# Optimization experiments

Hardware: AMD Instinct MI355X
Metric: run time of the kernel (lower is better)

The kernel has to match this reference:

```python
import jax, jax.numpy as jnp
import numpy as np

B, T, D = 4, 2048, 2048
P, K, ALPHA, R = 512, 16, 4, 32
E_RATIO = 0.8
EPS = 1e-6


def rmsnorm(x, g):
    return x * jax.lax.rsqrt(jnp.mean(x * x, axis=-1, keepdims=True) + EPS) * g


def dale_signs():
    # first e_ratio*P neurons excitatory (+1), rest inhibitory (-1)
    return jnp.where(jnp.arange(P) < int(E_RATIO * P), 1.0, -1.0)


def quant_dale(w, signs):
    # STE sign-quantization with per-neuron mean-abs scale + Dale's-law sign constraint
    scale = jnp.mean(jnp.abs(w), axis=-1, keepdims=True)  # [P,1]
    q = scale * signs[:, None] * jnp.ones_like(w)         # magnitude=scale, sign fixed per neuron
    return w + jax.lax.stop_gradient(q - w)


def synapse_graph(x, idx, w):
    # x: [B,T,D], idx: [P,K] int, w: [P,K] -> dendritic inputs [B,T,P,K]
    return jnp.take(x, idx, axis=-1) * w


def perceptron(x_dend, Wp, Wout, signs):
    Wq = quant_dale(Wp, signs)                              # [P,K]
    u = jnp.einsum('btpk,pk->btp', x_dend, Wq)              # [B,T,P]
    f = jax.nn.sigmoid(u)                                   # gate [B,T,P]
    f_out = quant_dale(Wout, signs)                         # [P,ALPHA]
    y = (f * u)[..., None] * f_out                          # [B,T,P,ALPHA]
    return u, f, y, f_out


def low_rank_ssm(t, f, s0, U, V, Wgate, bgate):
    # t,f: [B,T,P]; s0: [B,R]. Low-rank gated linear scan in R dims.
    z = jnp.einsum('btp,pr->btr', t, U)
    lam = jax.nn.sigmoid(jnp.einsum('btp,pr->btr', f, Wgate) + bgate)

    def step(s, inp):
        z_t, l_t = inp
        s = l_t * s + z_t
        return s, s

    sT, S = jax.lax.scan(step, s0, (jnp.moveaxis(z, 1, 0), jnp.moveaxis(lam, 1, 0)))
    tilde = jnp.einsum('btr,rp->btp', jnp.moveaxis(S, 0, 1), V)
    return tilde, sT


def flatten_ports(y):
    return y.reshape(*y.shape[:-2], P * ALPHA)


def setup_inputs() -> dict:
    key = jax.random.key(0)
    ks = jax.random.split(key, 14)
    sc = 0.1
    return {
        'x': jax.random.normal(ks[0], (B, T, D), jnp.float32),
        'state': jnp.zeros((B, R), jnp.float32),
        'g1': jnp.ones((D,), jnp.float32),
        'g2': jnp.ones((D,), jnp.float32),
        'idx_ssm': jax.random.randint(ks[1], (P, K), 0, D),
        'wg_ssm': jax.random.normal(ks[2], (P, K), jnp.float32) * sc,
        'idx_mlp': jax.random.randint(ks[3], (P, K), 0, D),
        'wg_mlp': jax.random.normal(ks[4], (P, K), jnp.float32) * sc,
        'Wp_ssm': jax.random.normal(ks[5], (P, K), jnp.float32) * sc,
        'Wout_ssm': jax.random.normal(ks[6], (P, ALPHA), jnp.float32) * sc,
        'Wp_mlp': jax.random.normal(ks[7], (P, K), jnp.float32) * sc,
        'Wout_mlp': jax.random.normal(ks[8], (P, ALPHA), jnp.float32) * sc,
        'U': jax.random.normal(ks[9], (P, R), jnp.float32) * sc,
        'V': jax.random.normal(ks[10], (R, P), jnp.float32) * sc,
        'Wgate': jax.random.normal(ks[11], (P, R), jnp.float32) * sc,
        'bgate': jnp.zeros((R,), jnp.float32),
    }


def reference(x, state, g1, g2, idx_ssm, wg_ssm, idx_mlp, wg_mlp,
              Wp_ssm, Wout_ssm, Wp_mlp, Wout_mlp, U, V, Wgate, bgate):
    signs = dale_signs()
    # --- SSM branch ---
    h1 = rmsnorm(x, g1)
    x_dend_ssm = synapse_graph(h1, idx_ssm, wg_ssm)
    u_ssm, f_ssm, _, f_out = perceptron(x_dend_ssm, Wp_ssm, Wout_ssm, signs)
    t_ssm = f_ssm * u_ssm
    tilde_t, new_state = low_rank_ssm(t_ssm, f_ssm, state, U, V, Wgate, bgate)
    y_ssm = (f_ssm * tilde_t)[..., None] * f_out            # [B,T,P,ALPHA]
    x_after = x + flatten_ports(y_ssm)
    # --- MLP branch ---
    h2 = rmsnorm(x_after, g2)
    x_dend_mlp = synapse_graph(h2, idx_mlp, wg_mlp)
    _, _, y_mlp, _ = perceptron(x_dend_mlp, Wp_mlp, Wout_mlp, signs)
    x_out = x_after + flatten_ports(y_mlp)
    return x_out, new_state
```

## Files before the change

### kernel.cpp

```cpp
#include <hip/hip_runtime.h>
#include <hip/hip_bf16.h>

#define B_ 4
#define T_ 2048
#define D_ 2048
#define P_ 512
#define K_ 16
#define ALPHA_ 4
#define R_ 32
#define NE_ 409
#define EPS_ 1e-6f
#define G_ 4

typedef unsigned short u16;

__device__ __forceinline__ float sigmoidf_(float x) {
  return 1.0f / (1.0f + __expf(-x));
}
__device__ __forceinline__ float bfb2f(u16 u) {
  return __uint_as_float(((unsigned int)u) << 16);
}
__device__ __forceinline__ u16 f2bfb(float f) {
  __hip_bfloat16 h = __float2bfloat16(f);
  return *reinterpret_cast<u16*>(&h);
}

__global__ void k_scalars(const float* __restrict__ Wp_s, const float* __restrict__ Wo_s,
                          const float* __restrict__ Wp_m, const float* __restrict__ Wo_m,
                          float* __restrict__ wq_s, float* __restrict__ fo_s,
                          float* __restrict__ wq_m, float* __restrict__ fo_m) {
  int p = blockIdx.x * blockDim.x + threadIdx.x;
  if (p >= P_) return;
  float sgn = (p < NE_) ? 1.0f : -1.0f;
  float a = 0, b = 0, c = 0, d = 0;
#pragma unroll
  for (int k = 0; k < K_; k++) {
    a += fabsf(Wp_s[p * K_ + k]);
    c += fabsf(Wp_m[p * K_ + k]);
  }
#pragma unroll
  for (int k = 0; k < ALPHA_; k++) {
    b += fabsf(Wo_s[p * ALPHA_ + k]);
    d += fabsf(Wo_m[p * ALPHA_ + k]);
  }
  wq_s[p] = sgn * a * (1.0f / K_);
  fo_s[p] = sgn * b * (1.0f / ALPHA_);
  wq_m[p] = sgn * c * (1.0f / K_);
  fo_m[p] = sgn * d * (1.0f / ALPHA_);
}

__global__ __launch_bounds__(256) void k_phase1(
    const float* __restrict__ x, const float* __restrict__ g1,
    const int* __restrict__ idx, const float* __restrict__ wg,
    const float* __restrict__ U, const float* __restrict__ Wgt,
    const float* __restrict__ bg, const float* __restrict__ wq,
    float* __restrict__ f_ssm, float* __restrict__ z, float* __restrict__ lam) {
  __shared__ u16 h1[G_][D_];
  __shared__ float fl[G_][P_];
  __shared__ float tl[G_][P_];
  __shared__ float red[G_][4];
  __shared__ float zp[G_][R_][4];
  __shared__ float lp[G_][R_][4];

  int tid = threadIdx.x;
  int token0 = blockIdx.x * G_;
  int b = token0 >> 11;
  int t0 = token0 & (T_ - 1);

  float gv[8];
  {
    const float4* gp = reinterpret_cast<const float4*>(g1 + tid * 8);
    *reinterpret_cast<float4*>(&gv[0]) = gp[0];
    *reinterpret_cast<float4*>(&gv[4]) = gp[1];
  }
  float xv[G_][8];
  float ssv[G_];
#pragma unroll
  for (int tok = 0; tok < G_; tok++) {
    const float4* xp = reinterpret_cast<const float4*>(x + (size_t)(token0 + tok) * D_ + tid * 8);
    *reinterpret_cast<float4*>(&xv[tok][0]) = xp[0];
    *reinterpret_cast<float4*>(&xv[tok][4]) = xp[1];
    float ss = 0;
#pragma unroll
    for (int i = 0; i < 8; i++) ss += xv[tok][i] * xv[tok][i];
    ssv[tok] = ss;
  }
#pragma unroll
  for (int tok = 0; tok < G_; tok++) {
    float s = ssv[tok];
#pragma unroll
    for (int off = 32; off; off >>= 1) s += __shfl_down(s, off);
    if ((tid & 63) == 0) red[tok][tid >> 6] = s;
  }
  __syncthreads();
#pragma unroll
  for (int tok = 0; tok < G_; tok++) {
    float inv = rsqrtf((red[tok][0] + red[tok][1] + red[tok][2] + red[tok][3]) * (1.0f / D_) + EPS_);
    u16 tmp[8];
#pragma unroll
    for (int i = 0; i < 8; i++) tmp[i] = f2bfb(xv[tok][i] * inv * gv[i]);
    *reinterpret_cast<uint4*>(&h1[tok][tid * 8]) = *reinterpret_cast<const uint4*>(tmp);
  }
  __syncthreads();

#pragma unroll
  for (int j = 0; j < 2; j++) {
    int p = tid + j * 256;
    union { int4 v[4]; int s[16]; } iu;
    const int4* ip = reinterpret_cast<const int4*>(idx + p * K_);
    iu.v[0] = ip[0]; iu.v[1] = ip[1]; iu.v[2] = ip[2]; iu.v[3] = ip[3];
    union { float4 v[4]; float s[16]; } wu;
    const float4* wp = reinterpret_cast<const float4*>(wg + p * K_);
    wu.v[0] = wp[0]; wu.v[1] = wp[1]; wu.v[2] = wp[2]; wu.v[3] = wp[3];
    float wqp = wq[p];
#pragma unroll
    for (int tok = 0; tok < G_; tok++) {
      float acc = 0;
#pragma unroll
      for (int k = 0; k < K_; k++) acc += bfb2f(h1[tok][iu.s[k]]) * wu.s[k];
      float u = wqp * acc;
      float f = sigmoidf_(u);
      fl[tok][p] = f;
      tl[tok][p] = f * u;
      f_ssm[(size_t)(token0 + tok) * P_ + p] = f;
    }
  }
  __syncthreads();

  int r = tid & 31, g = tid >> 5;
  float zs[G_], ls[G_];
#pragma unroll
  for (int tok = 0; tok < G_; tok++) { zs[tok] = 0; ls[tok] = 0; }
  int pbase = g * 64;
#pragma unroll 4
  for (int pp = 0; pp < 64; pp++) {
    int p = pbase + pp;
    float uu = U[p * R_ + r];
    float ww = Wgt[p * R_ + r];
#pragma unroll
    for (int tok = 0; tok < G_; tok++) {
      zs[tok] += tl[tok][p] * uu;
      ls[tok] += fl[tok][p] * ww;
    }
  }
#pragma unroll
  for (int tok = 0; tok < G_; tok++) {
    zs[tok] += __shfl_down(zs[tok], 32);
    ls[tok] += __shfl_down(ls[tok], 32);
  }
  int wid = tid >> 6;
  if ((tid & 32) == 0 && (tid & 63) < 32) {
#pragma unroll
    for (int tok = 0; tok < G_; tok++) {
      zp[tok][r][wid] = zs[tok];
      lp[tok][r][wid] = ls[tok];
    }
  }
  __syncthreads();
  if (tid < R_) {
    float bgr = bg[tid];
    float z4[G_], l4[G_];
#pragma unroll
    for (int tok = 0; tok < G_; tok++) {
      float zz = zp[tok][tid][0] + zp[tok][tid][1] + zp[tok][tid][2] + zp[tok][tid][3];
      float ll = lp[tok][tid][0] + lp[tok][tid][1] + lp[tok][tid][2] + lp[tok][tid][3];
      z4[tok] = zz;
      l4[tok] = sigmoidf_(ll + bgr);
    }
    size_t o = ((size_t)(b * R_ + tid)) * T_ + t0;
    *reinterpret_cast<float4*>(&z[o]) = *reinterpret_cast<const float4*>(z4);
    *reinterpret_cast<float4*>(&lam[o]) = *reinterpret_cast<const float4*>(l4);
  }
}

__global__ __launch_bounds__(64) void k_scan(
    const float* __restrict__ z, const float* __restrict__ lam,
    const float* __restrict__ state, float* __restrict__ S,
    float* __restrict__ out_state) {
  int br = blockIdx.x;
  int lane = threadIdx.x;
  const float* zr = z + (size_t)br * T_ + lane * 32;
  const float* lr = lam + (size_t)br * T_ + lane * 32;
  float zb[32], lb[32];
#pragma unroll
  for (int i = 0; i < 32; i += 4) {
    *reinterpret_cast<float4*>(&zb[i]) = *reinterpret_cast<const float4*>(&zr[i]);
    *reinterpret_cast<float4*>(&lb[i]) = *reinterpret_cast<const float4*>(&lr[i]);
  }
  float A = 1.0f, Z = 0.0f;
#pragma unroll
  for (int i = 0; i < 32; i++) { Z = lb[i] * Z + zb[i]; A *= lb[i]; }
  for (int off = 1; off < 64; off <<= 1) {
    float Ap = __shfl_up(A, off);
    float Zp = __shfl_up(Z, off);
    if (lane >= off) { Z = A * Zp + Z; A = A * Ap; }
  }
  float s0 = state[br];
  float Ae = __shfl_up(A, 1);
  float Ze = __shfl_up(Z, 1);
  float s = (lane == 0) ? s0 : (Ae * s0 + Ze);
  float sb[32];
#pragma unroll
  for (int i = 0; i < 32; i++) { s = lb[i] * s + zb[i]; sb[i] = s; }
  float* Sr = S + (size_t)br * T_ + lane * 32;
#pragma unroll
  for (int i = 0; i < 32; i += 4)
    *reinterpret_cast<float4*>(&Sr[i]) = *reinterpret_cast<const float4*>(&sb[i]);
  if (lane == 63) out_state[br] = s;
}

__global__ __launch_bounds__(256) void k_phase3(
    const float* __restrict__ x, const float* __restrict__ g2,
    const int* __restrict__ idx, const float* __restrict__ wg,
    const float* __restrict__ V, const float* __restrict__ S,
    const float* __restrict__ f_ssm, const float* __restrict__ fo_s,
    const float* __restrict__ wq_m, const float* __restrict__ fo_m,
    float* __restrict__ out) {
  __shared__ float Sl[G_][R_];
  __shared__ u16 h2[G_][D_];
  __shared__ float red[G_][4];

  int tid = threadIdx.x;
  int token0 = blockIdx.x * G_;
  int b = token0 >> 11;
  int t0 = token0 & (T_ - 1);

  if (tid < G_ * R_) {
    int tok = tid >> 5, r = tid & 31;
    Sl[tok][r] = S[((size_t)(b * R_ + r)) * T_ + t0 + tok];
  }
  __syncthreads();

  int p0 = 2 * tid, p1 = 2 * tid + 1;

  float til0[G_], til1[G_];
#pragma unroll
  for (int tok = 0; tok < G_; tok++) { til0[tok] = 0; til1[tok] = 0; }
#pragma unroll 4
  for (int r = 0; r < R_; r++) {
    float2 vv = *reinterpret_cast<const float2*>(V + r * P_ + p0);
#pragma unroll
    for (int tok = 0; tok < G_; tok++) {
      float s = Sl[tok][r];
      til0[tok] += s * vv.x;
      til1[tok] += s * vv.y;
    }
  }

  float2 fo = *reinterpret_cast<const float2*>(fo_s + p0);
  float gv[8];
  {
    const float4* gp = reinterpret_cast<const float4*>(g2 + tid * 8);
    *reinterpret_cast<float4*>(&gv[0]) = gp[0];
    *reinterpret_cast<float4*>(&gv[4]) = gp[1];
  }

  float xa[G_][8];
#pragma unroll
  for (int tok = 0; tok < G_; tok++) {
    float2 ff = *reinterpret_cast<const float2*>(f_ssm + (size_t)(token0 + tok) * P_ + p0);
    float val0 = ff.x * til0[tok] * fo.x;
    float val1 = ff.y * til1[tok] * fo.y;
    float xv[8];
    const float4* xp = reinterpret_cast<const float4*>(x + (size_t)(token0 + tok) * D_ + tid * 8);
    *reinterpret_cast<float4*>(&xv[0]) = xp[0];
    *reinterpret_cast<float4*>(&xv[4]) = xp[1];
    float ss = 0;
#pragma unroll
    for (int a = 0; a < 4; a++) {
      float v0 = xv[a] + val0;
      float v1 = xv[4 + a] + val1;
      xa[tok][a] = v0;
      xa[tok][4 + a] = v1;
      ss += v0 * v0 + v1 * v1;
    }
#pragma unroll
    for (int off = 32; off; off >>= 1) ss += __shfl_down(ss, off);
    if ((tid & 63) == 0) red[tok][tid >> 6] = ss;
  }
  __syncthreads();
#pragma unroll
  for (int tok = 0; tok < G_; tok++) {
    float inv = rsqrtf((red[tok][0] + red[tok][1] + red[tok][2] + red[tok][3]) * (1.0f / D_) + EPS_);
    u16 tmp[8];
#pragma unroll
    for (int i = 0; i < 8; i++) tmp[i] = f2bfb(xa[tok][i] * inv * gv[i]);
    *reinterpret_cast<uint4*>(&h2[tok][tid * 8]) = *reinterpret_cast<const uint4*>(tmp);
  }
  __syncthreads();

  union { int4 v[4]; int s[16]; } iu0, iu1;
  union { float4 v[4]; float s[16]; } wu0, wu1;
  {
    const int4* ip0 = reinterpret_cast<const int4*>(idx + p0 * K_);
    const int4* ip1 = reinterpret_cast<const int4*>(idx + p1 * K_);
    const float4* wp0 = reinterpret_cast<const float4*>(wg + p0 * K_);
    const float4* wp1 = reinterpret_cast<const float4*>(wg + p1 * K_);
#pragma unroll
    for (int q = 0; q < 4; q++) { iu0.v[q] = ip0[q]; iu1.v[q] = ip1[q]; wu0.v[q] = wp0[q]; wu1.v[q] = wp1[q]; }
  }
  float2 wqm = *reinterpret_cast<const float2*>(wq_m + p0);
  float2 fom = *reinterpret_cast<const float2*>(fo_m + p0);

#pragma unroll
  for (int tok = 0; tok < G_; tok++) {
    float acc0 = 0, acc1 = 0;
#pragma unroll
    for (int k = 0; k < K_; k++) {
      acc0 += bfb2f(h2[tok][iu0.s[k]]) * wu0.s[k];
      acc1 += bfb2f(h2[tok][iu1.s[k]]) * wu1.s[k];
    }
    float u0 = wqm.x * acc0, u1 = wqm.y * acc1;
    float f0 = sigmoidf_(u0), f1 = sigmoidf_(u1);
    float val0 = f0 * u0 * fom.x, val1 = f1 * u1 * fom.y;
    float ov[8];
#pragma unroll
    for (int a = 0; a < 4; a++) {
      ov[a] = xa[tok][a] + val0;
      ov[4 + a] = xa[tok][4 + a] + val1;
    }
    float4* op = reinterpret_cast<float4*>(out + (size_t)(token0 + tok) * D_ + tid * 8);
    op[0] = *reinterpret_cast<const float4*>(&ov[0]);
    op[1] = *reinterpret_cast<const float4*>(&ov[4]);
  }
}

extern "C" void kernel_launch(void* const* d_in, const int* in_sizes, int n_in,
                              void* d_out, int out_size, void* d_ws, size_t ws_size,
                              hipStream_t stream) {
  const float* x     = (const float*)d_in[0];
  const float* state = (const float*)d_in[1];
  const float* g1    = (const float*)d_in[2];
  const float* g2    = (const float*)d_in[3];
  const int*   idx_s = (const int*)d_in[4];
  const float* wg_s  = (const float*)d_in[5];
  const int*   idx_m = (const int*)d_in[6];
  const float* wg_m  = (const float*)d_in[7];
  const float* Wp_s  = (const float*)d_in[8];
  const float* Wo_s  = (const float*)d_in[9];
  const float* Wp_m  = (const float*)d_in[10];
  const float* Wo_m  = (const float*)d_in[11];
  const float* U     = (const float*)d_in[12];
  const float* V     = (const float*)d_in[13];
  const float* Wgt   = (const float*)d_in[14];
  const float* bg    = (const float*)d_in[15];
  float* out = (float*)d_out;

  char* ws = (char*)d_ws;
  float* wq_s = (float*)(ws + 0);
  float* fo_s = (float*)(ws + 2048);
  float* wq_m = (float*)(ws + 4096);
  float* fo_m = (float*)(ws + 6144);
  float* f_ssm = (float*)(ws + 8192);
  size_t off = 8192 + (size_t)B_ * T_ * P_ * 4;
  float* z   = (float*)(ws + off); off += (size_t)B_ * R_ * T_ * 4;
  float* lam = (float*)(ws + off); off += (size_t)B_ * R_ * T_ * 4;
  float* S   = (float*)(ws + off);

  hipLaunchKernelGGL(k_scalars, dim3(2), dim3(256), 0, stream,
                     Wp_s, Wo_s, Wp_m, Wo_m, wq_s, fo_s, wq_m, fo_m);
  hipLaunchKernelGGL(k_phase1, dim3(B_ * T_ / G_), dim3(256), 0, stream,
                     x, g1, idx_s, wg_s, U, Wgt, bg, wq_s, f_ssm, z, lam);
  hipLaunchKernelGGL(k_scan, dim3(B_ * R_), dim3(64), 0, stream,
                     z, lam, state, S, out + (size_t)B_ * T_ * D_);
  hipLaunchKernelGGL(k_phase3, dim3(B_ * T_ / G_), dim3(256), 0, stream,
                     x, g2, idx_m, wg_m, V, S, f_ssm, fo_s, wq_m, fo_m, out);
}
```

Before: 212.6 us.

## Fold weight-scale kernel into phases, defer RMS scale, store gate as bf16

Removes the separate k_scalars launch: each phase kernel now recomputes the Dale-quantized scales from the raw weights. The RMSnorm scale is applied after the gather instead of before, which removes one block barrier in both phase kernels. The f_ssm intermediate and the shared-memory t/f arrays are packed as bf16, which halves global and LDS traffic. The cost is redundant per-block scale arithmetic and extra bf16 rounding of the gate and gated values.

New measurement: 236.1 us. +11.0%, slower.

```diff
diff --git a/kernel.cpp b/kernel.cpp
--- a/kernel.cpp
+++ b/kernel.cpp
@@ -13,51 +13,29 @@
 #define G_ 4
 
 typedef unsigned short u16;
+typedef unsigned int u32;
 
 __device__ __forceinline__ float sigmoidf_(float x) {
   return 1.0f / (1.0f + __expf(-x));
 }
 __device__ __forceinline__ float bfb2f(u16 u) {
-  return __uint_as_float(((unsigned int)u) << 16);
+  return __uint_as_float(((u32)u) << 16);
 }
 __device__ __forceinline__ u16 f2bfb(float f) {
   __hip_bfloat16 h = __float2bfloat16(f);
   return *reinterpret_cast<u16*>(&h);
 }
-
-__global__ void k_scalars(const float* __restrict__ Wp_s, const float* __restrict__ Wo_s,
-                          const float* __restrict__ Wp_m, const float* __restrict__ Wo_m,
-                          float* __restrict__ wq_s, float* __restrict__ fo_s,
-                          float* __restrict__ wq_m, float* __restrict__ fo_m) {
-  int p = blockIdx.x * blockDim.x + threadIdx.x;
-  if (p >= P_) return;
-  float sgn = (p < NE_) ? 1.0f : -1.0f;
-  float a = 0, b = 0, c = 0, d = 0;
-#pragma unroll
-  for (int k = 0; k < K_; k++) {
-    a += fabsf(Wp_s[p * K_ + k]);
-    c += fabsf(Wp_m[p * K_ + k]);
-  }
-#pragma unroll
-  for (int k = 0; k < ALPHA_; k++) {
-    b += fabsf(Wo_s[p * ALPHA_ + k]);
-    d += fabsf(Wo_m[p * ALPHA_ + k]);
-  }
-  wq_s[p] = sgn * a * (1.0f / K_);
-  fo_s[p] = sgn * b * (1.0f / ALPHA_);
-  wq_m[p] = sgn * c * (1.0f / K_);
-  fo_m[p] = sgn * d * (1.0f / ALPHA_);
-}
+__device__ __forceinline__ float bflo(u32 u) { return __uint_as_float(u << 16); }
+__device__ __forceinline__ float bfhi(u32 u) { return __uint_as_float(u & 0xFFFF0000u); }
 
 __global__ __launch_bounds__(256) void k_phase1(
     const float* __restrict__ x, const float* __restrict__ g1,
     const int* __restrict__ idx, const float* __restrict__ wg,
-    const float* __restrict__ U, const float* __restrict__ Wgt,
-    const float* __restrict__ bg, const float* __restrict__ wq,
-    float* __restrict__ f_ssm, float* __restrict__ z, float* __restrict__ lam) {
+    const float* __restrict__ Wp, const float* __restrict__ U,
+    const float* __restrict__ Wgt, const float* __restrict__ bg,
+    u16* __restrict__ f_ssm, float* __restrict__ z, float* __restrict__ lam) {
   __shared__ u16 h1[G_][D_];
-  __shared__ float fl[G_][P_];
-  __shared__ float tl[G_][P_];
+  __shared__ u32 tf[G_][P_];
   __shared__ float red[G_][4];
   __shared__ float zp[G_][R_][4];
   __shared__ float lp[G_][R_][4];
@@ -73,35 +51,27 @@
     *reinterpret_cast<float4*>(&gv[0]) = gp[0];
     *reinterpret_cast<float4*>(&gv[4]) = gp[1];
   }
-  float xv[G_][8];
-  float ssv[G_];
-#pragma unroll
-  for (int tok = 0; tok < G_; tok++) {
+#pragma unroll
+  for (int tok = 0; tok < G_; tok++) {
+    float xv[8];
     const float4* xp = reinterpret_cast<const float4*>(x + (size_t)(token0 + tok) * D_ + tid * 8);
-    *reinterpret_cast<float4*>(&xv[tok][0]) = xp[0];
-    *reinterpret_cast<float4*>(&xv[tok][4]) = xp[1];
+    *reinterpret_cast<float4*>(&xv[0]) = xp[0];
+    *reinterpret_cast<float4*>(&xv[4]) = xp[1];
     float ss = 0;
-#pragma unroll
-    for (int i = 0; i < 8; i++) ss += xv[tok][i] * xv[tok][i];
-    ssv[tok] = ss;
-  }
-#pragma unroll
-  for (int tok = 0; tok < G_; tok++) {
-    float s = ssv[tok];
-#pragma unroll
-    for (int off = 32; off; off >>= 1) s += __shfl_down(s, off);
-    if ((tid & 63) == 0) red[tok][tid >> 6] = s;
-  }
-  __syncthreads();
-#pragma unroll
-  for (int tok = 0; tok < G_; tok++) {
-    float inv = rsqrtf((red[tok][0] + red[tok][1] + red[tok][2] + red[tok][3]) * (1.0f / D_) + EPS_);
     u16 tmp[8];
 #pragma unroll
-    for (int i = 0; i < 8; i++) tmp[i] = f2bfb(xv[tok][i] * inv * gv[i]);
+    for (int i = 0; i < 8; i++) { ss += xv[i] * xv[i]; tmp[i] = f2bfb(xv[i] * gv[i]); }
     *reinterpret_cast<uint4*>(&h1[tok][tid * 8]) = *reinterpret_cast<const uint4*>(tmp);
-  }
-  __syncthreads();
+#pragma unroll
+    for (int off = 32; off; off >>= 1) ss += __shfl_down(ss, off);
+    if ((tid & 63) == 0) red[tok][tid >> 6] = ss;
+  }
+  __syncthreads();
+
+  float inv[G_];
+#pragma unroll
+  for (int tok = 0; tok < G_; tok++)
+    inv[tok] = rsqrtf((red[tok][0] + red[tok][1] + red[tok][2] + red[tok][3]) * (1.0f / D_) + EPS_);
 
 #pragma unroll
   for (int j = 0; j < 2; j++) {
@@ -112,17 +82,25 @@
     union { float4 v[4]; float s[16]; } wu;
     const float4* wp = reinterpret_cast<const float4*>(wg + p * K_);
     wu.v[0] = wp[0]; wu.v[1] = wp[1]; wu.v[2] = wp[2]; wu.v[3] = wp[3];
-    float wqp = wq[p];
+    float aw = 0;
+    {
+      const float4* qp = reinterpret_cast<const float4*>(Wp + p * K_);
+#pragma unroll
+      for (int q = 0; q < 4; q++) {
+        float4 w = qp[q];
+        aw += fabsf(w.x) + fabsf(w.y) + fabsf(w.z) + fabsf(w.w);
+      }
+    }
+    float wqp = ((p < NE_) ? 1.0f : -1.0f) * aw * (1.0f / K_);
 #pragma unroll
     for (int tok = 0; tok < G_; tok++) {
       float acc = 0;
 #pragma unroll
       for (int k = 0; k < K_; k++) acc += bfb2f(h1[tok][iu.s[k]]) * wu.s[k];
-      float u = wqp * acc;
+      float u = wqp * inv[tok] * acc;
       float f = sigmoidf_(u);
-      fl[tok][p] = f;
-      tl[tok][p] = f * u;
-      f_ssm[(size_t)(token0 + tok) * P_ + p] = f;
+      tf[tok][p] = ((u32)f2bfb(f) << 16) | (u32)f2bfb(f * u);
+      f_ssm[(size_t)(token0 + tok) * P_ + p] = f2bfb(f);
     }
   }
   __syncthreads();
@@ -131,16 +109,19 @@
   float zs[G_], ls[G_];
 #pragma unroll
   for (int tok = 0; tok < G_; tok++) { zs[tok] = 0; ls[tok] = 0; }
-  int pbase = g * 64;
-#pragma unroll 4
-  for (int pp = 0; pp < 64; pp++) {
-    int p = pbase + pp;
-    float uu = U[p * R_ + r];
-    float ww = Wgt[p * R_ + r];
+  int pb = g * 64;
+#pragma unroll 2
+  for (int pq = 0; pq < 16; pq++) {
+    int p = pb + pq * 4;
+    float u0 = U[(p + 0) * R_ + r], u1 = U[(p + 1) * R_ + r];
+    float u2 = U[(p + 2) * R_ + r], u3 = U[(p + 3) * R_ + r];
+    float w0 = Wgt[(p + 0) * R_ + r], w1 = Wgt[(p + 1) * R_ + r];
+    float w2 = Wgt[(p + 2) * R_ + r], w3 = Wgt[(p + 3) * R_ + r];
 #pragma unroll
     for (int tok = 0; tok < G_; tok++) {
-      zs[tok] += tl[tok][p] * uu;
-      ls[tok] += fl[tok][p] * ww;
+      uint4 q = *reinterpret_cast<const uint4*>(&tf[tok][p]);
+      zs[tok] += bflo(q.x) * u0 + bflo(q.y) * u1 + bflo(q.z) * u2 + bflo(q.w) * u3;
+      ls[tok] += bfhi(q.x) * w0 + bfhi(q.y) * w1 + bfhi(q.z) * w2 + bfhi(q.w) * w3;
     }
   }
 #pragma unroll
@@ -149,12 +130,9 @@
     ls[tok] += __shfl_down(ls[tok], 32);
   }
   int wid = tid >> 6;
-  if ((tid & 32) == 0 && (tid & 63) < 32) {
-#pragma unroll
-    for (int tok = 0; tok < G_; tok++) {
-      zp[tok][r][wid] = zs[tok];
-      lp[tok][r][wid] = ls[tok];
-    }
+  if ((tid & 63) < 32) {
+#pragma unroll
+    for (int tok = 0; tok < G_; tok++) { zp[tok][r][wid] = zs[tok]; lp[tok][r][wid] = ls[tok]; }
   }
   __syncthreads();
   if (tid < R_) {
@@ -212,9 +190,9 @@
 __global__ __launch_bounds__(256) void k_phase3(
     const float* __restrict__ x, const float* __restrict__ g2,
     const int* __restrict__ idx, const float* __restrict__ wg,
-    const float* __restrict__ V, const float* __restrict__ S,
-    const float* __restrict__ f_ssm, const float* __restrict__ fo_s,
-    const float* __restrict__ wq_m, const float* __restrict__ fo_m,
+    const float* __restrict__ Wo_s, const float* __restrict__ Wp_m,
+    const float* __restrict__ Wo_m, const float* __restrict__ V,
+    const float* __restrict__ S, const u16* __restrict__ f_ssm,
     float* __restrict__ out) {
   __shared__ float Sl[G_][R_];
   __shared__ u16 h2[G_][D_];
@@ -224,100 +202,131 @@
   int token0 = blockIdx.x * G_;
   int b = token0 >> 11;
   int t0 = token0 & (T_ - 1);
+  int p0 = 2 * tid;
 
   if (tid < G_ * R_) {
     int tok = tid >> 5, r = tid & 31;
     Sl[tok][r] = S[((size_t)(b * R_ + r)) * T_ + t0 + tok];
   }
-  __syncthreads();
-
-  int p0 = 2 * tid, p1 = 2 * tid + 1;
-
-  float til0[G_], til1[G_];
-#pragma unroll
-  for (int tok = 0; tok < G_; tok++) { til0[tok] = 0; til1[tok] = 0; }
-#pragma unroll 4
-  for (int r = 0; r < R_; r++) {
-    float2 vv = *reinterpret_cast<const float2*>(V + r * P_ + p0);
-#pragma unroll
-    for (int tok = 0; tok < G_; tok++) {
-      float s = Sl[tok][r];
-      til0[tok] += s * vv.x;
-      til1[tok] += s * vv.y;
-    }
-  }
-
-  float2 fo = *reinterpret_cast<const float2*>(fo_s + p0);
+
   float gv[8];
   {
     const float4* gp = reinterpret_cast<const float4*>(g2 + tid * 8);
     *reinterpret_cast<float4*>(&gv[0]) = gp[0];
     *reinterpret_cast<float4*>(&gv[4]) = gp[1];
   }
-
-  float xa[G_][8];
-#pragma unroll
-  for (int tok = 0; tok < G_; tok++) {
-    float2 ff = *reinterpret_cast<const float2*>(f_ssm + (size_t)(token0 + tok) * P_ + p0);
-    float val0 = ff.x * til0[tok] * fo.x;
-    float val1 = ff.y * til1[tok] * fo.y;
-    float xv[8];
+  float xv[G_][8];
+#pragma unroll
+  for (int tok = 0; tok < G_; tok++) {
     const float4* xp = reinterpret_cast<const float4*>(x + (size_t)(token0 + tok) * D_ + tid * 8);
-    *reinterpret_cast<float4*>(&xv[0]) = xp[0];
-    *reinterpret_cast<float4*>(&xv[4]) = xp[1];
-    float ss = 0;
-#pragma unroll
-    for (int a = 0; a < 4; a++) {
-      float v0 = xv[a] + val0;
-      float v1 = xv[4 + a] + val1;
-      xa[tok][a] = v0;
-      xa[tok][4 + a] = v1;
-      ss += v0 * v0 + v1 * v1;
-    }
-#pragma unroll
-    for (int off = 32; off; off >>= 1) ss += __shfl_down(ss, off);
-    if ((tid & 63) == 0) red[tok][tid >> 6] = ss;
-  }
-  __syncthreads();
-#pragma unroll
-  for (int tok = 0; tok < G_; tok++) {
-    float inv = rsqrtf((red[tok][0] + red[tok][1] + red[tok][2] + red[tok][3]) * (1.0f / D_) + EPS_);
-    u16 tmp[8];
-#pragma unroll
-    for (int i = 0; i < 8; i++) tmp[i] = f2bfb(xa[tok][i] * inv * gv[i]);
-    *reinterpret_cast<uint4*>(&h2[tok][tid * 8]) = *reinterpret_cast<const uint4*>(tmp);
-  }
-  __syncthreads();
+    *reinterpret_cast<float4*>(&xv[tok][0]) = xp[0];
+    *reinterpret_cast<float4*>(&xv[tok][4]) = xp[1];
+  }
+  u32 fb[G_];
+#pragma unroll
+  for (int tok = 0; tok < G_; tok++)
+    fb[tok] = *reinterpret_cast<const u32*>(f_ssm + (size_t)(token0 + tok) * P_ + p0);
+
+  float sgn0 = (p0 < NE_) ? 1.0f : -1.0f;
+  float sgn1 = (p0 + 1 < NE_) ? 1.0f : -1.0f;
+  float fo0, fo1, fom0, fom1, wqm0, wqm1;
+  {
+    float4 a = *reinterpret_cast<const float4*>(Wo_s + p0 * ALPHA_);
+    float4 c = *reinterpret_cast<const float4*>(Wo_s + (p0 + 1) * ALPHA_);
+    fo0 = sgn0 * 0.25f * (fabsf(a.x) + fabsf(a.y) + fabsf(a.z) + fabsf(a.w));
+    fo1 = sgn1 * 0.25f * (fabsf(c.x) + fabsf(c.y) + fabsf(c.z) + fabsf(c.w));
+    float4 e = *reinterpret_cast<const float4*>(Wo_m + p0 * ALPHA_);
+    float4 h = *reinterpret_cast<const float4*>(Wo_m + (p0 + 1) * ALPHA_);
+    fom0 = sgn0 * 0.25f * (fabsf(e.x) + fabsf(e.y) + fabsf(e.z) + fabsf(e.w));
+    fom1 = sgn1 * 0.25f * (fabsf(h.x) + fabsf(h.y) + fabsf(h.z) + fabsf(h.w));
+    float aw0 = 0, aw1 = 0;
+    const float4* q0 = reinterpret_cast<const float4*>(Wp_m + p0 * K_);
+    const float4* q1 = reinterpret_cast<const float4*>(Wp_m + (p0 + 1) * K_);
+#pragma unroll
+    for (int q = 0; q < 4; q++) {
+      float4 wa = q0[q], wb = q1[q];
+      aw0 += fabsf(wa.x) + fabsf(wa.y) + fabsf(wa.z) + fabsf(wa.w);
+      aw1 += fabsf(wb.x) + fabsf(wb.y) + fabsf(wb.z) + fabsf(wb.w);
+    }
+    wqm0 = sgn0 * aw0 * (1.0f / K_);
+    wqm1 = sgn1 * aw1 * (1.0f / K_);
+  }
+  __syncthreads();
+
+  float til0[G_], til1[G_];
+#pragma unroll
+  for (int tok = 0; tok < G_; tok++) { til0[tok] = 0; til1[tok] = 0; }
+  const float2* V2 = reinterpret_cast<const float2*>(V);
+#pragma unroll
+  for (int rq = 0; rq < 8; rq++) {
+    float4 sq[G_];
+#pragma unroll
+    for (int tok = 0; tok < G_; tok++)
+      sq[tok] = *reinterpret_cast<const float4*>(&Sl[tok][rq * 4]);
+#pragma unroll
+    for (int i = 0; i < 4; i++) {
+      float2 vv = V2[(size_t)(rq * 4 + i) * (P_ / 2) + tid];
+#pragma unroll
+      for (int tok = 0; tok < G_; tok++) {
+        float s = (i == 0) ? sq[tok].x : (i == 1) ? sq[tok].y : (i == 2) ? sq[tok].z : sq[tok].w;
+        til0[tok] += s * vv.x;
+        til1[tok] += s * vv.y;
+      }
+    }
+  }
 
   union { int4 v[4]; int s[16]; } iu0, iu1;
   union { float4 v[4]; float s[16]; } wu0, wu1;
   {
     const int4* ip0 = reinterpret_cast<const int4*>(idx + p0 * K_);
-    const int4* ip1 = reinterpret_cast<const int4*>(idx + p1 * K_);
+    const int4* ip1 = reinterpret_cast<const int4*>(idx + (p0 + 1) * K_);
     const float4* wp0 = reinterpret_cast<const float4*>(wg + p0 * K_);
-    const float4* wp1 = reinterpret_cast<const float4*>(wg + p1 * K_);
+    const float4* wp1 = reinterpret_cast<const float4*>(wg + (p0 + 1) * K_);
 #pragma unroll
     for (int q = 0; q < 4; q++) { iu0.v[q] = ip0[q]; iu1.v[q] = ip1[q]; wu0.v[q] = wp0[q]; wu1.v[q] = wp1[q]; }
   }
-  float2 wqm = *reinterpret_cast<const float2*>(wq_m + p0);
-  float2 fom = *reinterpret_cast<const float2*>(fo_m + p0);
-
-#pragma unroll
-  for (int tok = 0; tok < G_; tok++) {
+
+#pragma unroll
+  for (int tok = 0; tok < G_; tok++) {
+    float f0 = bflo(fb[tok]), f1 = bfhi(fb[tok]);
+    float val0 = f0 * til0[tok] * fo0;
+    float val1 = f1 * til1[tok] * fo1;
+    float ss = 0;
+#pragma unroll
+    for (int a = 0; a < 4; a++) {
+      float v0 = xv[tok][a] + val0;
+      float v1 = xv[tok][4 + a] + val1;
+      xv[tok][a] = v0;
+      xv[tok][4 + a] = v1;
+      ss += v0 * v0 + v1 * v1;
+    }
+    u16 tmp[8];
+#pragma unroll
+    for (int i = 0; i < 8; i++) tmp[i] = f2bfb(xv[tok][i] * gv[i]);
+    *reinterpret_cast<uint4*>(&h2[tok][tid * 8]) = *reinterpret_cast<const uint4*>(tmp);
+#pragma unroll
+    for (int off = 32; off; off >>= 1) ss += __shfl_down(ss, off);
+    if ((tid & 63) == 0) red[tok][tid >> 6] = ss;
+  }
+  __syncthreads();
+
+#pragma unroll
+  for (int tok = 0; tok < G_; tok++) {
+    float invt = rsqrtf((red[tok][0] + red[tok][1] + red[tok][2] + red[tok][3]) * (1.0f / D_) + EPS_);
     float acc0 = 0, acc1 = 0;
 #pragma unroll
     for (int k = 0; k < K_; k++) {
       acc0 += bfb2f(h2[tok][iu0.s[k]]) * wu0.s[k];
       acc1 += bfb2f(h2[tok][iu1.s[k]]) * wu1.s[k];
     }
-    float u0 = wqm.x * acc0, u1 = wqm.y * acc1;
+    float u0 = wqm0 * invt * acc0, u1 = wqm1 * invt * acc1;
     float f0 = sigmoidf_(u0), f1 = sigmoidf_(u1);
-    float val0 = f0 * u0 * fom.x, val1 = f1 * u1 * fom.y;
+    float val0 = f0 * u0 * fom0, val1 = f1 * u1 * fom1;
     float ov[8];
 #pragma unroll
     for (int a = 0; a < 4; a++) {
-      ov[a] = xa[tok][a] + val0;
-      ov[4 + a] = xa[tok][4 + a] + val1;
+      ov[a] = xv[tok][a] + val0;
+      ov[4 + a] = xv[tok][4 + a] + val1;
     }
     float4* op = reinterpret_cast<float4*>(out + (size_t)(token0 + tok) * D_ + tid * 8);
     op[0] = *reinterpret_cast<const float4*>(&ov[0]);
@@ -347,22 +356,16 @@
   float* out = (float*)d_out;
 
   char* ws = (char*)d_ws;
-  float* wq_s = (float*)(ws + 0);
-  float* fo_s = (float*)(ws + 2048);
-  float* wq_m = (float*)(ws + 4096);
-  float* fo_m = (float*)(ws + 6144);
-  float* f_ssm = (float*)(ws + 8192);
-  size_t off = 8192 + (size_t)B_ * T_ * P_ * 4;
+  u16* f_ssm = (u16*)ws;
+  size_t off = (size_t)B_ * T_ * P_ * 2;
   float* z   = (float*)(ws + off); off += (size_t)B_ * R_ * T_ * 4;
   float* lam = (float*)(ws + off); off += (size_t)B_ * R_ * T_ * 4;
   float* S   = (float*)(ws + off);
 
-  hipLaunchKernelGGL(k_scalars, dim3(2), dim3(256), 0, stream,
-                     Wp_s, Wo_s, Wp_m, Wo_m, wq_s, fo_s, wq_m, fo_m);
   hipLaunchKernelGGL(k_phase1, dim3(B_ * T_ / G_), dim3(256), 0, stream,
-                     x, g1, idx_s, wg_s, U, Wgt, bg, wq_s, f_ssm, z, lam);
+                     x, g1, idx_s, wg_s, Wp_s, U, Wgt, bg, f_ssm, z, lam);
   hipLaunchKernelGGL(k_scan, dim3(B_ * R_), dim3(64), 0, stream,
                      z, lam, state, S, out + (size_t)B_ * T_ * D_);
   hipLaunchKernelGGL(k_phase3, dim3(B_ * T_ / G_), dim3(256), 0, stream,
-                     x, g2, idx_m, wg_m, V, S, f_ssm, fo_s, wq_m, fo_m, out);
-}
+                     x, g2, idx_m, wg_m, Wo_s, Wp_m, Wo_m, V, S, f_ssm, out);
+}
```

## Store f_ssm in bf16, defer RMS scale past gather, pack gate data

Applied to the files above, without the earlier changes.

The f_ssm intermediate is now stored as bf16 instead of fp32, which halves its round trip through global memory between phase1 and phase3. In both phases the RMS normalization factor is applied after the sparse gather-dot rather than to every element before the bf16 store. This removes one block barrier and the extra pass over registers. In phase1, f and f*u are packed together as bf16 pairs in shared memory, and the U/Wgate and V loops are restructured to use vectorized shared reads. The cost is extra rounding of f, t and the unscaled h values, which shifts numerics.

Result: no change. 215.2 us (+1.2%).

```diff
diff --git a/kernel.cpp b/kernel.cpp
--- a/kernel.cpp
+++ b/kernel.cpp
@@ -13,17 +13,20 @@
 #define G_ 4
 
 typedef unsigned short u16;
+typedef unsigned int u32;
 
 __device__ __forceinline__ float sigmoidf_(float x) {
   return 1.0f / (1.0f + __expf(-x));
 }
 __device__ __forceinline__ float bfb2f(u16 u) {
-  return __uint_as_float(((unsigned int)u) << 16);
+  return __uint_as_float(((u32)u) << 16);
 }
 __device__ __forceinline__ u16 f2bfb(float f) {
   __hip_bfloat16 h = __float2bfloat16(f);
   return *reinterpret_cast<u16*>(&h);
 }
+__device__ __forceinline__ float bflo(u32 u) { return __uint_as_float(u << 16); }
+__device__ __forceinline__ float bfhi(u32 u) { return __uint_as_float(u & 0xFFFF0000u); }
 
 __global__ void k_scalars(const float* __restrict__ Wp_s, const float* __restrict__ Wo_s,
                           const float* __restrict__ Wp_m, const float* __restrict__ Wo_m,
@@ -54,10 +57,9 @@
     const int* __restrict__ idx, const float* __restrict__ wg,
     const float* __restrict__ U, const float* __restrict__ Wgt,
     const float* __restrict__ bg, const float* __restrict__ wq,
-    float* __restrict__ f_ssm, float* __restrict__ z, float* __restrict__ lam) {
+    u16* __restrict__ f_ssm, float* __restrict__ z, float* __restrict__ lam) {
   __shared__ u16 h1[G_][D_];
-  __shared__ float fl[G_][P_];
-  __shared__ float tl[G_][P_];
+  __shared__ u32 tf[G_][P_];
   __shared__ float red[G_][4];
   __shared__ float zp[G_][R_][4];
   __shared__ float lp[G_][R_][4];
@@ -73,35 +75,27 @@
     *reinterpret_cast<float4*>(&gv[0]) = gp[0];
     *reinterpret_cast<float4*>(&gv[4]) = gp[1];
   }
-  float xv[G_][8];
-  float ssv[G_];
 #pragma unroll
   for (int tok = 0; tok < G_; tok++) {
+    float xv[8];
     const float4* xp = reinterpret_cast<const float4*>(x + (size_t)(token0 + tok) * D_ + tid * 8);
-    *reinterpret_cast<float4*>(&xv[tok][0]) = xp[0];
-    *reinterpret_cast<float4*>(&xv[tok][4]) = xp[1];
+    *reinterpret_cast<float4*>(&xv[0]) = xp[0];
+    *reinterpret_cast<float4*>(&xv[4]) = xp[1];
     float ss = 0;
-#pragma unroll
-    for (int i = 0; i < 8; i++) ss += xv[tok][i] * xv[tok][i];
-    ssv[tok] = ss;
-  }
-#pragma unroll
-  for (int tok = 0; tok < G_; tok++) {
-    float s = ssv[tok];
-#pragma unroll
-    for (int off = 32; off; off >>= 1) s += __shfl_down(s, off);
-    if ((tid & 63) == 0) red[tok][tid >> 6] = s;
-  }
-  __syncthreads();
-#pragma unroll
-  for (int tok = 0; tok < G_; tok++) {
-    float inv = rsqrtf((red[tok][0] + red[tok][1] + red[tok][2] + red[tok][3]) * (1.0f / D_) + EPS_);
     u16 tmp[8];
 #pragma unroll
-    for (int i = 0; i < 8; i++) tmp[i] = f2bfb(xv[tok][i] * inv * gv[i]);
+    for (int i = 0; i < 8; i++) { ss += xv[i] * xv[i]; tmp[i] = f2bfb(xv[i] * gv[i]); }
     *reinterpret_cast<uint4*>(&h1[tok][tid * 8]) = *reinterpret_cast<const uint4*>(tmp);
-  }
-  __syncthreads();
+#pragma unroll
+    for (int off = 32; off; off >>= 1) ss += __shfl_down(ss, off);
+    if ((tid & 63) == 0) red[tok][tid >> 6] = ss;
+  }
+  __syncthreads();
+
+  float inv[G_];
+#pragma unroll
+  for (int tok = 0; tok < G_; tok++)
+    inv[tok] = rsqrtf((red[tok][0] + red[tok][1] + red[tok][2] + red[tok][3]) * (1.0f / D_) + EPS_);
 
 #pragma unroll
   for (int j = 0; j < 2; j++) {
@@ -118,11 +112,10 @@
       float acc = 0;
 #pragma unroll
       for (int k = 0; k < K_; k++) acc += bfb2f(h1[tok][iu.s[k]]) * wu.s[k];
-      float u = wqp * acc;
+      float u = wqp * inv[tok] * acc;
       float f = sigmoidf_(u);
-      fl[tok][p] = f;
-      tl[tok][p] = f * u;
-      f_ssm[(size_t)(token0 + tok) * P_ + p] = f;
+      tf[tok][p] = ((u32)f2bfb(f) << 16) | (u32)f2bfb(f * u);
+      f_ssm[(size_t)(token0 + tok) * P_ + p] = f2bfb(f);
     }
   }
   __syncthreads();
@@ -131,16 +124,19 @@
   float zs[G_], ls[G_];
 #pragma unroll
   for (int tok = 0; tok < G_; tok++) { zs[tok] = 0; ls[tok] = 0; }
-  int pbase = g * 64;
-#pragma unroll 4
-  for (int pp = 0; pp < 64; pp++) {
-    int p = pbase + pp;
-    float uu = U[p * R_ + r];
-    float ww = Wgt[p * R_ + r];
+  int pb = g * 64;
+#pragma unroll 2
+  for (int pq = 0; pq < 16; pq++) {
+    int p = pb + pq * 4;
+    float u0 = U[(p + 0) * R_ + r], u1 = U[(p + 1) * R_ + r];
+    float u2 = U[(p + 2) * R_ + r], u3 = U[(p + 3) * R_ + r];
+    float w0 = Wgt[(p + 0) * R_ + r], w1 = Wgt[(p + 1) * R_ + r];
+    float w2 = Wgt[(p + 2) * R_ + r], w3 = Wgt[(p + 3) * R_ + r];
 #pragma unroll
     for (int tok = 0; tok < G_; tok++) {
-      zs[tok] += tl[tok][p] * uu;
-      ls[tok] += fl[tok][p] * ww;
+      uint4 q = *reinterpret_cast<const uint4*>(&tf[tok][p]);
+      zs[tok] += bflo(q.x) * u0 + bflo(q.y) * u1 + bflo(q.z) * u2 + bflo(q.w) * u3;
+      ls[tok] += bfhi(q.x) * w0 + bfhi(q.y) * w1 + bfhi(q.z) * w2 + bfhi(q.w) * w3;
     }
   }
 #pragma unroll
@@ -149,12 +145,9 @@
     ls[tok] += __shfl_down(ls[tok], 32);
   }
   int wid = tid >> 6;
-  if ((tid & 32) == 0 && (tid & 63) < 32) {
-#pragma unroll
-    for (int tok = 0; tok < G_; tok++) {
-      zp[tok][r][wid] = zs[tok];
-      lp[tok][r][wid] = ls[tok];
-    }
+  if ((tid & 63) < 32) {
+#pragma unroll
+    for (int tok = 0; tok < G_; tok++) { zp[tok][r][wid] = zs[tok]; lp[tok][r][wid] = ls[tok]; }
   }
   __syncthreads();
   if (tid < R_) {
@@ -213,7 +206,7 @@
     const float* __restrict__ x, const float* __restrict__ g2,
     const int* __restrict__ idx, const float* __restrict__ wg,
     const float* __restrict__ V, const float* __restrict__ S,
-    const float* __restrict__ f_ssm, const float* __restrict__ fo_s,
+    const u16* __restrict__ f_ssm, const float* __restrict__ fo_s,
     const float* __restrict__ wq_m, const float* __restrict__ fo_m,
     float* __restrict__ out) {
   __shared__ float Sl[G_][R_];
@@ -224,6 +217,7 @@
   int token0 = blockIdx.x * G_;
   int b = token0 >> 11;
   int t0 = token0 & (T_ - 1);
+  int p0 = 2 * tid;
 
   if (tid < G_ * R_) {
     int tok = tid >> 5, r = tid & 31;
@@ -231,19 +225,25 @@
   }
   __syncthreads();
 
-  int p0 = 2 * tid, p1 = 2 * tid + 1;
-
   float til0[G_], til1[G_];
 #pragma unroll
   for (int tok = 0; tok < G_; tok++) { til0[tok] = 0; til1[tok] = 0; }
-#pragma unroll 4
-  for (int r = 0; r < R_; r++) {
-    float2 vv = *reinterpret_cast<const float2*>(V + r * P_ + p0);
-#pragma unroll
-    for (int tok = 0; tok < G_; tok++) {
-      float s = Sl[tok][r];
-      til0[tok] += s * vv.x;
-      til1[tok] += s * vv.y;
+  const float2* V2 = reinterpret_cast<const float2*>(V);
+#pragma unroll
+  for (int rq = 0; rq < 8; rq++) {
+    float4 sq[G_];
+#pragma unroll
+    for (int tok = 0; tok < G_; tok++)
+      sq[tok] = *reinterpret_cast<const float4*>(&Sl[tok][rq * 4]);
+#pragma unroll
+    for (int i = 0; i < 4; i++) {
+      float2 vv = V2[(size_t)(rq * 4 + i) * (P_ / 2) + tid];
+#pragma unroll
+      for (int tok = 0; tok < G_; tok++) {
+        float s = (i == 0) ? sq[tok].x : (i == 1) ? sq[tok].y : (i == 2) ? sq[tok].z : sq[tok].w;
+        til0[tok] += s * vv.x;
+        til1[tok] += s * vv.y;
+      }
     }
   }
 
@@ -258,9 +258,9 @@
   float xa[G_][8];
 #pragma unroll
   for (int tok = 0; tok < G_; tok++) {
-    float2 ff = *reinterpret_cast<const float2*>(f_ssm + (size_t)(token0 + tok) * P_ + p0);
-    float val0 = ff.x * til0[tok] * fo.x;
-    float val1 = ff.y * til1[tok] * fo.y;
+    u32 ff = *reinterpret_cast<const u32*>(f_ssm + (size_t)(token0 + tok) * P_ + p0);
+    float val0 = bflo(ff) * til0[tok] * fo.x;
+    float val1 = bfhi(ff) * til1[tok] * fo.y;
     float xv[8];
     const float4* xp = reinterpret_cast<const float4*>(x + (size_t)(token0 + tok) * D_ + tid * 8);
     *reinterpret_cast<float4*>(&xv[0]) = xp[0];
@@ -274,18 +274,13 @@
       xa[tok][4 + a] = v1;
       ss += v0 * v0 + v1 * v1;
     }
+    u16 tmp[8];
+#pragma unroll
+    for (int i = 0; i < 8; i++) tmp[i] = f2bfb(xa[tok][i] * gv[i]);
+    *reinterpret_cast<uint4*>(&h2[tok][tid * 8]) = *reinterpret_cast<const uint4*>(tmp);
 #pragma unroll
     for (int off = 32; off; off >>= 1) ss += __shfl_down(ss, off);
     if ((tid & 63) == 0) red[tok][tid >> 6] = ss;
-  }
-  __syncthreads();
-#pragma unroll
-  for (int tok = 0; tok < G_; tok++) {
-    float inv = rsqrtf((red[tok][0] + red[tok][1] + red[tok][2] + red[tok][3]) * (1.0f / D_) + EPS_);
-    u16 tmp[8];
-#pragma unroll
-    for (int i = 0; i < 8; i++) tmp[i] = f2bfb(xa[tok][i] * inv * gv[i]);
-    *reinterpret_cast<uint4*>(&h2[tok][tid * 8]) = *reinterpret_cast<const uint4*>(tmp);
   }
   __syncthreads();
 
@@ -293,9 +288,9 @@
   union { float4 v[4]; float s[16]; } wu0, wu1;
   {
     const int4* ip0 = reinterpret_cast<const int4*>(idx + p0 * K_);
-    const int4* ip1 = reinterpret_cast<const int4*>(idx + p1 * K_);
+    const int4* ip1 = reinterpret_cast<const int4*>(idx + (p0 + 1) * K_);
     const float4* wp0 = reinterpret_cast<const float4*>(wg + p0 * K_);
-    const float4* wp1 = reinterpret_cast<const float4*>(wg + p1 * K_);
+    const float4* wp1 = reinterpret_cast<const float4*>(wg + (p0 + 1) * K_);
 #pragma unroll
     for (int q = 0; q < 4; q++) { iu0.v[q] = ip0[q]; iu1.v[q] = ip1[q]; wu0.v[q] = wp0[q]; wu1.v[q] = wp1[q]; }
   }
@@ -304,13 +299,14 @@
 
 #pragma unroll
   for (int tok = 0; tok < G_; tok++) {
+    float invt = rsqrtf((red[tok][0] + red[tok][1] + red[tok][2] + red[tok][3]) * (1.0f / D_) + EPS_);
     float acc0 = 0, acc1 = 0;
 #pragma unroll
     for (int k = 0; k < K_; k++) {
       acc0 += bfb2f(h2[tok][iu0.s[k]]) * wu0.s[k];
       acc1 += bfb2f(h2[tok][iu1.s[k]]) * wu1.s[k];
     }
-    float u0 = wqm.x * acc0, u1 = wqm.y * acc1;
+    float u0 = wqm.x * invt * acc0, u1 = wqm.y * invt * acc1;
     float f0 = sigmoidf_(u0), f1 = sigmoidf_(u1);
     float val0 = f0 * u0 * fom.x, val1 = f1 * u1 * fom.y;
     float ov[8];
@@ -351,8 +347,8 @@
   float* fo_s = (float*)(ws + 2048);
   float* wq_m = (float*)(ws + 4096);
   float* fo_m = (float*)(ws + 6144);
-  float* f_ssm = (float*)(ws + 8192);
-  size_t off = 8192 + (size_t)B_ * T_ * P_ * 4;
+  u16* f_ssm = (u16*)(ws + 8192);
+  size_t off = 8192 + (size_t)B_ * T_ * P_ * 2;
   float* z   = (float*)(ws + off); off += (size_t)B_ * R_ * T_ * 4;
   float* lam = (float*)(ws + off); off += (size_t)B_ * R_ * T_ * 4;
   float* S   = (float*)(ws + off);
```
